# Optimization experiments

Measured on AMD Instinct MI355X. Metric: run time of the kernel, lower is better.

The kernel has to match this reference:

```python
import jax, jax.numpy as jnp
import numpy as np

N_HEADS = 8
N_POINTS = 4
LN_EPS = 1e-5


def _ln(x, g, b):
    m = jnp.mean(x, -1, keepdims=True)
    v = jnp.mean((x - m) ** 2, -1, keepdims=True)
    return (x - m) * jax.lax.rsqrt(v + LN_EPS) * g + b


def _mha(q, k, v, wq, bq, wk, bk, wv, bv, wo, bo):
    B, Lq, C = q.shape
    Dh = C // N_HEADS
    Q = (q @ wq.T + bq).reshape(B, Lq, N_HEADS, Dh)
    K = (k @ wk.T + bk).reshape(B, -1, N_HEADS, Dh)
    V = (v @ wv.T + bv).reshape(B, -1, N_HEADS, Dh)
    s = jnp.einsum('bqhd,bkhd->bhqk', Q, K) * (1.0 / float(np.sqrt(Dh)))
    a = jax.nn.softmax(s, -1)
    o = jnp.einsum('bhqk,bkhd->bqhd', a, V).reshape(B, Lq, C)
    return o @ wo.T + bo


def _ref_points(h, w, L):
    ry = jnp.linspace(0.5, h - 0.5, h) / h
    rx = jnp.linspace(0.5, w - 0.5, w) / w
    gy, gx = jnp.meshgrid(ry, rx, indexing='ij')
    ref = jnp.stack([gx.reshape(-1), gy.reshape(-1)], -1)[None]  # (1, h*w, 2)
    return jnp.broadcast_to(ref[:, :, None, :], (1, h * w, L, 2))


def _deform_core(value, shapes, starts, loc, aw):
    # value: (B, Len_in, H, Dh); loc: (B, Lq, H, L, P, 2); aw: (B, Lq, H, L, P)
    B, _, H, Dh = value.shape
    Lq, P = loc.shape[1], loc.shape[4]
    out = jnp.zeros((B, H, Lq, Dh), value.dtype)
    for l in range(shapes.shape[0]):
        Hl, Wl = int(shapes[l, 0]), int(shapes[l, 1])
        s = int(starts[l])
        v = value[:, s:s + Hl * Wl].transpose(0, 2, 1, 3)  # (B, H, Hl*Wl, Dh)
        # grid_sample(align_corners=False, padding_mode='zeros') pixel coords
        xl = loc[:, :, :, l, :, 0] * Wl - 0.5  # (B, Lq, H, P)
        yl = loc[:, :, :, l, :, 1] * Hl - 0.5
        x0 = jnp.floor(xl); y0 = jnp.floor(yl)
        fx = xl - x0; fy = yl - y0
        x0 = x0.astype(jnp.int32); y0 = y0.astype(jnp.int32)
        acc = jnp.zeros((B, H, Lq, P, Dh), value.dtype)
        for dy, dx in ((0, 0), (0, 1), (1, 0), (1, 1)):
            xi = x0 + dx; yi = y0 + dy
            wgt = (fx if dx else 1.0 - fx) * (fy if dy else 1.0 - fy)
            valid = ((xi >= 0) & (xi < Wl) & (yi >= 0) & (yi < Hl)).astype(value.dtype)
            idx = (jnp.clip(yi, 0, Hl - 1) * Wl + jnp.clip(xi, 0, Wl - 1))
            idx = idx.transpose(0, 2, 1, 3).reshape(B, H, Lq * P)
            g = jnp.take_along_axis(v, idx[..., None], axis=2).reshape(B, H, Lq, P, Dh)
            acc = acc + g * (wgt * valid).transpose(0, 2, 1, 3)[..., None]
        out = out + jnp.einsum('bhqpd,bqhp->bhqd', acc, aw[:, :, :, l])
    return out.transpose(0, 2, 1, 3).reshape(B, Lq, H * Dh)


def reference(tgt, query_pos, src, wq, bq, wk, bk, wv, bv, wo, bo, ln2_g, ln2_b,
              w_off, b_off, w_attn, b_attn, w_val, b_val, w_cout, b_cout,
              ln1_g, ln1_b, w1, b1, w2, b2, ln3_g, ln3_b,
              src_spatial_shapes, level_start_index, h, w):
    shapes = np.asarray(src_spatial_shapes)
    starts = np.asarray(level_start_index)
    h = int(h); w = int(w)
    L = shapes.shape[0]
    B, Lq, C = tgt.shape
    Dh = C // N_HEADS
    # --- self attention (post-LN residual) ---
    q = tgt + query_pos
    t2 = _mha(q, q, tgt, wq, bq, wk, bk, wv, bv, wo, bo)
    t = _ln(tgt + t2, ln2_g, ln2_b)
    # --- MSDeformAttn cross attention ---
    qc = t + query_pos
    value = (src @ w_val.T + b_val).reshape(B, -1, N_HEADS, Dh)
    off = (qc @ w_off.T + b_off).reshape(B, Lq, N_HEADS, L, N_POINTS, 2)
    aw = (qc @ w_attn.T + b_attn).reshape(B, Lq, N_HEADS, L * N_POINTS)
    aw = jax.nn.softmax(aw, -1).reshape(B, Lq, N_HEADS, L, N_POINTS)
    norm = jnp.stack([shapes[:, 1].astype(np.float32), shapes[:, 0].astype(np.float32)], -1)  # (L,2): (W,H)
    rp = _ref_points(h, w, L)  # (1, Lq, L, 2)
    loc = rp[:, :, None, :, None, :] + off / norm[None, None, None, :, None, :]
    samp = _deform_core(value, shapes, starts, loc, aw)
    t2 = samp @ w_cout.T + b_cout
    t = _ln(t + t2, ln1_g, ln1_b)
    # --- FFN ---
    t2 = jax.nn.relu(t @ w1.T + b1) @ w2.T + b2
    t = _ln(t + t2, ln3_g, ln3_b)
    return t


def setup_inputs() -> dict:
    key = jax.random.key(0)
    B, C, L, P, dff = 2, 256, 4, 4, 1024
    h = w = 48
    shapes = np.array([[48, 48], [24, 24], [12, 12], [6, 6]], np.int32)
    starts = np.array([0, 2304, 2880, 3024], np.int32)
    Len_in = 3060
    Lq = h * w
    ks = iter(jax.random.split(key, 40))
    def rn(shape, s=0.02):
        return jax.random.normal(next(ks), shape, jnp.float32) * s
    return dict(
        tgt=rn((B, Lq, C), 1.0), query_pos=rn((B, Lq, C), 1.0), src=rn((B, Len_in, C), 1.0),
        wq=rn((C, C)), bq=rn((C,)), wk=rn((C, C)), bk=rn((C,)), wv=rn((C, C)), bv=rn((C,)),
        wo=rn((C, C)), bo=rn((C,)),
        ln2_g=jnp.ones((C,)), ln2_b=jnp.zeros((C,)),
        w_off=rn((N_HEADS * L * P * 2, C)), b_off=rn((N_HEADS * L * P * 2,)),
        w_attn=rn((N_HEADS * L * P, C)), b_attn=rn((N_HEADS * L * P,)),
        w_val=rn((C, C)), b_val=rn((C,)), w_cout=rn((C, C)), b_cout=rn((C,)),
        ln1_g=jnp.ones((C,)), ln1_b=jnp.zeros((C,)),
        w1=rn((dff, C)), b1=rn((dff,)), w2=rn((C, dff)), b2=rn((C,)),
        ln3_g=jnp.ones((C,)), ln3_b=jnp.zeros((C,)),
        src_spatial_shapes=shapes, level_start_index=starts, h=h, w=w)
```

## Files before the change

kernel.cpp:

```cpp
#include <hip/hip_runtime.h>
#include <hip/hip_bf16.h>
#include <math.h>

typedef __hip_bfloat16 bf16;
typedef __attribute__((ext_vector_type(8))) short short8;
typedef __attribute__((ext_vector_type(4))) short short4v;
typedef __attribute__((ext_vector_type(4))) float f32x4;

static constexpr int B   = 2;
static constexpr int LQ  = 2304;
static constexpr int C   = 256;
static constexpr int NH  = 8;
static constexpr int DH  = 32;
static constexpr int NL  = 4;
static constexpr int NP  = 4;
static constexpr int LEN = 3060;
static constexpr int DFF = 1024;
static constexpr int MQ  = B * LQ;
static constexpr int MV  = B * LEN;
static constexpr int SZ1 = MQ * C;

#define MFMA16(a, b, c) __builtin_amdgcn_mfma_f32_16x16x32_bf16(a, b, c, 0, 0, 0)

__device__ __forceinline__ float ldf(const void* p, size_t i, int bf) {
  return bf ? __bfloat162float(((const bf16*)p)[i]) : ((const float*)p)[i];
}
__device__ __forceinline__ short fl2s(float v) {
  bf16 h = __float2bfloat16(v);
  return *(short*)&h;
}
__device__ __forceinline__ short fl2s_fast(float v) {
  union { float f; unsigned u; } x; x.f = v;
  return (short)((x.u + 0x8000u) >> 16);
}
__device__ __forceinline__ float s2fl(short s) {
  return __bfloat162float(*(bf16*)&s);
}
__device__ __forceinline__ int wire_is_bf16(const unsigned* gprobe) {
  return gprobe[0] == 0x3F803F80u;
}
__device__ __forceinline__ short8 add2bf(short8 a, short8 b) {
  short8 r;
#pragma unroll
  for (int j = 0; j < 8; ++j) r[j] = fl2s(s2fl(a[j]) + s2fl(b[j]));
  return r;
}

static constexpr int CVN = 20;
__device__ const int g_cvt_cnt[CVN] = {
  65536, 65536, 256, 256, 65536, 256, 65536, 256,
  65536, 32768, 256, 128, 65536, 256, 65536, 256,
  262144, 1024, 262144, 256};
__device__ const int g_cvt_off[CVN] = {
  0, 65536, 131072, 131328, 131584, 197120, 197376, 262912,
  263168, 328704, 361472, 361728, 361856, 427392, 427648, 493184,
  493440, 755584, 756608, 1018752};
static constexpr int CV_WQ = 0, CV_WK = 65536, CV_BQ = 131072, CV_BK = 131328;
static constexpr int CV_WV = 131584, CV_BV = 197120;
static constexpr int CV_WO = 197376, CV_BO = 262912;
static constexpr int CV_WOFF = 263168, CV_WATTN = 328704;
static constexpr int CV_BOFF = 361472, CV_BATTN = 361728;
static constexpr int CV_WVAL = 361856, CV_BVAL = 427392;
static constexpr int CV_WCOUT = 427648, CV_BCOUT = 493184;
static constexpr int CV_W1 = 493440, CV_B1 = 755584;
static constexpr int CV_W2 = 756608, CV_B2 = 1018752;
static constexpr int CV_TOTAL = 1019008;

struct CvtArgs { const void* p[22]; };

__global__ __launch_bounds__(256) void prep_all(CvtArgs a, const void* __restrict__ qpos,
                                                short* __restrict__ cvt,
                                                short* __restrict__ tgt16,
                                                short* __restrict__ q16,
                                                short* __restrict__ src16,
                                                const unsigned* __restrict__ gprobe) {
  if (wire_is_bf16(gprobe)) return;
  const int seg = blockIdx.y;
  const int cnt = (seg < 20) ? g_cvt_cnt[seg] : (seg == 20 ? SZ1 : MV * C);
  const int stride = gridDim.x * 256;
  for (int i = blockIdx.x * 256 + threadIdx.x; i < cnt; i += stride) {
    if (seg < 20) {
      cvt[g_cvt_off[seg] + i] = fl2s(((const float*)a.p[seg])[i]);
    } else if (seg == 20) {
      float t = ((const float*)a.p[20])[i];
      tgt16[i] = fl2s(t);
      q16[i] = fl2s(t + ((const float*)qpos)[i]);
    } else {
      src16[i] = fl2s(((const float*)a.p[21])[i]);
    }
  }
}

struct GemmJob {
  int Xmode;
  const short* Xbf; const void* Xwire; const void* Xwire2;
  const short* Wcvt; const short* bcvt;
  const void* Wwire; const void* bwire;
  void* Y;
  int M, N, K, ldY, col0, relu, out_mode, nblk_x;
  float qscale;
};
struct GemmBatch { GemmJob j[4]; int start[5]; int njobs; };

template <int MR>
__global__ __launch_bounds__(256) void gemm_mfma(GemmBatch nb,
                                                 const unsigned* __restrict__ gprobe) {
  constexpr int MT = MR / 64;
  const int fl = wire_is_bf16(gprobe);
  int id = blockIdx.x;
  int jj = 0;
  while (jj + 1 < nb.njobs && id >= nb.start[jj + 1]) ++jj;
  const GemmJob jb = nb.j[jj];
  const bool qcf = (jb.Xmode == 4) && fl;
  const short* Xsel = jb.Xbf;
  if ((jb.Xmode == 2 || jb.Xmode == 3) && fl) Xsel = (const short*)jb.Xwire;
  const short* Wsel = fl ? (const short*)jb.Wwire : jb.Wcvt;
  const short* bsel = fl ? (const short*)jb.bwire : jb.bcvt;
  const int local = id - nb.start[jj];
  const int bx = local % jb.nblk_x;
  const int by = local / jb.nblk_x;
  const int M = jb.M, N = jb.N, K = jb.K;

  __shared__ short Xs[MR][72];
  __shared__ short Ws[64][72];
  const int tid = threadIdx.x;
  const int wave = tid >> 6, lane = tid & 63;
  const int quad = lane >> 4, l16 = lane & 15;
  const int m0 = bx * MR, n0 = by * 64;
  f32x4 acc[MT][4];
#pragma unroll
  for (int mt = 0; mt < MT; ++mt)
#pragma unroll
    for (int nt = 0; nt < 4; ++nt) acc[mt][nt] = f32x4{0.f, 0.f, 0.f, 0.f};

  const int xrow = (MR == 128) ? (tid >> 1) : (tid >> 2);
  const int xcol = (MR == 128) ? ((tid & 1) * 32) : ((tid & 3) * 16);
  constexpr int XU = (MR == 128) ? 4 : 2;
  const int wrow = tid >> 2;
  const int wcol = (tid & 3) * 16;
  int xr = m0 + xrow; if (xr >= M) xr = M - 1;
  const short* xp = qcf ? nullptr : (Xsel + (size_t)xr * K);
  const short* tp = qcf ? ((const short*)jb.Xwire + (size_t)xr * K) : nullptr;
  const short* pp = qcf ? ((const short*)jb.Xwire2 + (size_t)xr * K) : nullptr;
  const short* wp = Wsel + (size_t)(n0 + wrow) * K;

  for (int k0 = 0; k0 < K; k0 += 64) {
    if (qcf) {
#pragma unroll
      for (int u = 0; u < XU; ++u) {
        short8 t8 = *(const short8*)(tp + k0 + xcol + u * 8);
        short8 p8 = *(const short8*)(pp + k0 + xcol + u * 8);
        *(short8*)&Xs[xrow][xcol + u * 8] = add2bf(t8, p8);
      }
    } else {
#pragma unroll
      for (int u = 0; u < XU; ++u)
        *(short8*)&Xs[xrow][xcol + u * 8] = *(const short8*)(xp + k0 + xcol + u * 8);
    }
    *(short8*)&Ws[wrow][wcol]     = *(const short8*)(wp + k0 + wcol);
    *(short8*)&Ws[wrow][wcol + 8] = *(const short8*)(wp + k0 + wcol + 8);
    __syncthreads();
#pragma unroll
    for (int kc = 0; kc < 2; ++kc) {
#pragma unroll
      for (int mt = 0; mt < MT; ++mt) {
        short8 a = *(const short8*)&Xs[wave * (16 * MT) + mt * 16 + l16][kc * 32 + quad * 8];
#pragma unroll
        for (int nt = 0; nt < 4; ++nt) {
          short8 b = *(const short8*)&Ws[nt * 16 + l16][kc * 32 + quad * 8];
          acc[mt][nt] = MFMA16(a, b, acc[mt][nt]);
        }
      }
    }
    __syncthreads();
  }

  if (jb.out_mode == 2) {
#pragma unroll
    for (int mt = 0; mt < MT; ++mt) {
      const int mbase = m0 + wave * (16 * MT) + mt * 16 + quad * 4;
      const int b = mbase / LQ;
      const int qb_ = mbase - b * LQ;
#pragma unroll
      for (int nt = 0; nt < 4; ++nt) {
        const int n = n0 + nt * 16 + l16;
        const float bv = s2fl(bsel[n]);
        short4v v4;
#pragma unroll
        for (int r = 0; r < 4; ++r) v4[r] = fl2s(acc[mt][nt][r] + bv);
        *(short4v*)((short*)jb.Y + (size_t)(b * 256 + n) * LQ + qb_) = v4;
      }
    }
    return;
  }
#pragma unroll
  for (int mt = 0; mt < MT; ++mt)
#pragma unroll
    for (int nt = 0; nt < 4; ++nt) {
      const int n = n0 + nt * 16 + l16;
      const float bv = s2fl(bsel[n]);
#pragma unroll
      for (int r = 0; r < 4; ++r) {
        const int m = m0 + wave * (16 * MT) + mt * 16 + quad * 4 + r;
        if (m < M) {
          float v = (acc[mt][nt][r] + bv) * jb.qscale;
          if (jb.relu) v = fmaxf(v, 0.f);
          if (jb.out_mode == 1)
            ((short*)jb.Y)[(size_t)m * jb.ldY + jb.col0 + n] = fl2s(v);
          else
            ((float*)jb.Y)[(size_t)m * jb.ldY + jb.col0 + n] = v;
        }
      }
    }
}

struct LnGemmArgs {
  const short* X;
  const short* Wcvt; const short* bcvt;
  const void* Wwire; const void* bwire;
  const void* R; int Rmode;
  const void* g; const void* be;
  float* Yf32; short* Y16; void* Yfinal;
  const void* pos; short* Yqc;
  int K;
};

__global__ __launch_bounds__(256) void gemm_ln(LnGemmArgs a,
                                               const unsigned* __restrict__ gprobe) {
  const int fl = wire_is_bf16(gprobe);
  const short* Wsel = fl ? (const short*)a.Wwire : a.Wcvt;
  const short* bsel = fl ? (const short*)a.bwire : a.bcvt;
  const int K = a.K;

  __shared__ short Xs[32][72];
  __shared__ short Ws[256][72];
  __shared__ float red[4][32][2];
  __shared__ float minv[32][2];

  const int tid = threadIdx.x;
  const int wave = tid >> 6, lane = tid & 63;
  const int quad = lane >> 4, l16 = lane & 15;
  const int m0 = blockIdx.x * 32;

  f32x4 acc[2][4];
#pragma unroll
  for (int mt = 0; mt < 2; ++mt)
#pragma unroll
    for (int nt = 0; nt < 4; ++nt) acc[mt][nt] = f32x4{0.f, 0.f, 0.f, 0.f};

  const int xrow = tid >> 3, xcol = (tid & 7) * 8;
  const int wrow = tid >> 2, wcol = (tid & 3) * 16;
  const short* xp = a.X + (size_t)(m0 + xrow) * K + xcol;

  for (int k0 = 0; k0 < K; k0 += 64) {
    *(short8*)&Xs[xrow][xcol] = *(const short8*)(xp + k0);
#pragma unroll
    for (int u = 0; u < 4; ++u) {
      const short* wp = Wsel + (size_t)(u * 64 + wrow) * K + k0 + wcol;
      *(short8*)&Ws[u * 64 + wrow][wcol]     = *(const short8*)(wp);
      *(short8*)&Ws[u * 64 + wrow][wcol + 8] = *(const short8*)(wp + 8);
    }
    __syncthreads();
#pragma unroll
    for (int kc = 0; kc < 2; ++kc)
#pragma unroll
      for (int mt = 0; mt < 2; ++mt) {
        short8 av = *(const short8*)&Xs[mt * 16 + l16][kc * 32 + quad * 8];
#pragma unroll
        for (int nt = 0; nt < 4; ++nt) {
          short8 bv = *(const short8*)&Ws[wave * 64 + nt * 16 + l16][kc * 32 + quad * 8];
          acc[mt][nt] = MFMA16(av, bv, acc[mt][nt]);
        }
      }
    __syncthreads();
  }

  float gc[4], bc[4], bb[4];
#pragma unroll
  for (int nt = 0; nt < 4; ++nt) {
    const int n = wave * 64 + nt * 16 + l16;
    gc[nt] = ldf(a.g, n, fl);
    bc[nt] = ldf(a.be, n, fl);
    bb[nt] = s2fl(bsel[n]);
  }
#pragma unroll
  for (int mt = 0; mt < 2; ++mt)
#pragma unroll
    for (int r = 0; r < 4; ++r) {
      const int rloc = mt * 16 + quad * 4 + r;
      const size_t row = (size_t)(m0 + rloc);
      float s = 0.f, s2 = 0.f;
#pragma unroll
      for (int nt = 0; nt < 4; ++nt) {
        const int n = wave * 64 + nt * 16 + l16;
        const size_t idx = row * C + n;
        const float rv = (a.Rmode == 1) ? ldf(a.R, idx, fl) : ((const float*)a.R)[idx];
        const float v = acc[mt][nt][r] + bb[nt] + rv;
        acc[mt][nt][r] = v;
        s += v;
        s2 += v * v;
      }
#pragma unroll
      for (int off = 8; off > 0; off >>= 1) {
        s  += __shfl_xor(s, off);
        s2 += __shfl_xor(s2, off);
      }
      if (l16 == 0) { red[wave][rloc][0] = s; red[wave][rloc][1] = s2; }
    }
  __syncthreads();
  if (tid < 32) {
    const float s  = red[0][tid][0] + red[1][tid][0] + red[2][tid][0] + red[3][tid][0];
    const float s2 = red[0][tid][1] + red[1][tid][1] + red[2][tid][1] + red[3][tid][1];
    const float mean = s * (1.f / C);
    const float var = fmaxf(s2 * (1.f / C) - mean * mean, 0.f);
    minv[tid][0] = mean;
    minv[tid][1] = rsqrtf(var + 1e-5f);
  }
  __syncthreads();
#pragma unroll
  for (int mt = 0; mt < 2; ++mt)
#pragma unroll
    for (int r = 0; r < 4; ++r) {
      const int rloc = mt * 16 + quad * 4 + r;
      const size_t row = (size_t)(m0 + rloc);
      const float mean = minv[rloc][0], inv = minv[rloc][1];
#pragma unroll
      for (int nt = 0; nt < 4; ++nt) {
        const int n = wave * 64 + nt * 16 + l16;
        const size_t idx = row * C + n;
        const float y = (acc[mt][nt][r] - mean) * inv * gc[nt] + bc[nt];
        if (a.Yfinal) {
          if (fl) ((short*)a.Yfinal)[idx] = fl2s(y);
          else    ((float*)a.Yfinal)[idx] = y;
        } else {
          if (a.Yf32) a.Yf32[idx] = y;
          if (a.Y16)  a.Y16[idx] = fl2s(y);
          if (a.Yqc)  a.Yqc[idx] = fl2s(y + ldf(a.pos, idx, fl));
        }
      }
    }
}

__global__ __launch_bounds__(256) void flash_attn(const short* __restrict__ QK,
                                                  const short* __restrict__ Vt,
                                                  short* __restrict__ Op) {
  constexpr int LDQK = 512;
  constexpr int NC = LQ / 64;
  constexpr int NQT = 3;
  const int qb = blockIdx.x;
  const int bh = blockIdx.y;
  const int b = bh >> 3, h = bh & 7;
  const int tid = threadIdx.x;
  const int wave = tid >> 6, lane = tid & 63;
  const int quad = lane >> 4, l16 = lane & 15;

  __shared__ short Ps[4][16][68];
  __shared__ float lsh[256];

  const int q0 = qb * 48;
  const size_t rowb = (size_t)(b * LQ);
  const short* kcol = QK + 256 + h * DH + quad * 8;
  const short* vt0 = Vt + (size_t)(b * 256 + h * 32 + l16) * LQ + quad * 8;
  const short* vt1 = Vt + (size_t)(b * 256 + h * 32 + 16 + l16) * LQ + quad * 8;

  short8 qfrag[NQT];
#pragma unroll
  for (int qt = 0; qt < NQT; ++qt)
    qfrag[qt] = *(const short8*)(QK + (rowb + q0 + qt * 16 + l16) * LDQK + h * DH + quad * 8);

  f32x4 o0[NQT], o1[NQT];
  float lrow[NQT];
#pragma unroll
  for (int qt = 0; qt < NQT; ++qt) {
    o0[qt] = f32x4{0.f, 0.f, 0.f, 0.f};
    o1[qt] = f32x4{0.f, 0.f, 0.f, 0.f};
    lrow[qt] = 0.f;
  }

  short8 kf[4], vf[4];
  {
    const int k0 = wave * 64;
#pragma unroll
    for (int kt = 0; kt < 4; ++kt)
      kf[kt] = *(const short8*)(kcol + (rowb + k0 + kt * 16 + l16) * LDQK);
    vf[0] = *(const short8*)(vt0 + k0);
    vf[1] = *(const short8*)(vt0 + k0 + 32);
    vf[2] = *(const short8*)(vt1 + k0);
    vf[3] = *(const short8*)(vt1 + k0 + 32);
  }

  for (int c = wave; c < NC; c += 4) {
    short8 kn[4], vn[4];
    if (c + 4 < NC) {
      const int k0n = (c + 4) * 64;
#pragma unroll
      for (int kt = 0; kt < 4; ++kt)
        kn[kt] = *(const short8*)(kcol + (rowb + k0n + kt * 16 + l16) * LDQK);
      vn[0] = *(const short8*)(vt0 + k0n);
      vn[1] = *(const short8*)(vt0 + k0n + 32);
      vn[2] = *(const short8*)(vt1 + k0n);
      vn[3] = *(const short8*)(vt1 + k0n + 32);
    }

#pragma unroll
    for (int qt = 0; qt < NQT; ++qt) {
      f32x4 s[4];
#pragma unroll
      for (int kt = 0; kt < 4; ++kt) {
        f32x4 z = {0.f, 0.f, 0.f, 0.f};
        s[kt] = MFMA16(kf[kt], qfrag[qt], z);
      }

      float ps = 0.f;
#pragma unroll
      for (int kt = 0; kt < 4; ++kt)
#pragma unroll
        for (int r = 0; r < 4; ++r) {
          float p = __expf(s[kt][r]);
          s[kt][r] = p;
          ps += p;
        }
      lrow[qt] += ps;

#pragma unroll
      for (int kt = 0; kt < 4; ++kt) {
        short4v pk;
#pragma unroll
        for (int r = 0; r < 4; ++r) pk[r] = fl2s_fast(s[kt][r]);
        *(short4v*)&Ps[wave][l16][kt * 16 + quad * 4] = pk;
      }

#pragma unroll
      for (int half = 0; half < 2; ++half) {
        short4v a0 = *(const short4v*)&Ps[wave][l16][half * 32 + quad * 8];
        short4v a1 = *(const short4v*)&Ps[wave][l16][half * 32 + quad * 8 + 4];
        short8 afrag;
#pragma unroll
        for (int j = 0; j < 4; ++j) { afrag[j] = a0[j]; afrag[4 + j] = a1[j]; }
        o0[qt] = MFMA16(afrag, vf[half], o0[qt]);
        o1[qt] = MFMA16(afrag, vf[2 + half], o1[qt]);
      }
    }

#pragma unroll
    for (int kt = 0; kt < 4; ++kt) { kf[kt] = kn[kt]; vf[kt] = vn[kt]; }
  }

  float* obuf = (float*)&Ps[0][0][0];
  for (int qt = 0; qt < NQT; ++qt) {
    __syncthreads();
    lsh[(wave * 4 + quad) * 16 + l16] = lrow[qt];
#pragma unroll
    for (int r = 0; r < 4; ++r) {
      const int q = quad * 4 + r;
      obuf[(wave * 16 + q) * 32 + l16] = o0[qt][r];
      obuf[(wave * 16 + q) * 32 + 16 + l16] = o1[qt][r];
    }
    __syncthreads();
#pragma unroll
    for (int e = tid; e < 512; e += 256) {
      const int q = e >> 5, d = e & 31;
      float lg = 0.f;
#pragma unroll
      for (int i = 0; i < 16; ++i) lg += lsh[i * 16 + q];
      float ov = 0.f;
#pragma unroll
      for (int w = 0; w < 4; ++w) ov += obuf[(w * 16 + q) * 32 + d];
      Op[(rowb + q0 + qt * 16 + q) * C + h * DH + d] = fl2s_fast(ov / lg);
    }
  }
}

__global__ __launch_bounds__(256) void deform_kern(const short* __restrict__ value,
                                                   const float* __restrict__ oa,
                                                   const int* __restrict__ shapes,
                                                   const int* __restrict__ starts,
                                                   const int* __restrict__ hp,
                                                   const int* __restrict__ wp,
                                                   short* __restrict__ samp) {
  const int bq = blockIdx.x * 4 + (threadIdx.x >> 6);
  const int b = bq / LQ, q = bq % LQ;
  const int lane = threadIdx.x & 63;
  const int h_ = lane >> 3;
  const int d0 = (lane & 7) * 4;

  const int w0 = *wp, h0 = *hp;
  const int qx = q % w0, qy = q / w0;
  const float refx = (qx + 0.5f) / (float)w0;
  const float refy = (qy + 0.5f) / (float)h0;

  const float* offp = oa + (size_t)bq * 384 + h_ * 32;
  const float* awraw = oa + (size_t)bq * 384 + 256 + h_ * 16;

  float e[16];
  float mm = -1e30f;
#pragma unroll
  for (int j = 0; j < 16; ++j) mm = fmaxf(mm, awraw[j]);
  float ssum = 0.f;
#pragma unroll
  for (int j = 0; j < 16; ++j) {
    e[j] = __expf(awraw[j] - mm);
    ssum += e[j];
  }
  const float sinv = 1.f / ssum;

  float acc0 = 0.f, acc1 = 0.f, acc2 = 0.f, acc3 = 0.f;
  for (int l = 0; l < NL; ++l) {
    const int Hl = shapes[l * 2 + 0];
    const int Wl = shapes[l * 2 + 1];
    const int st = starts[l];
    const short* vbase = value + ((size_t)(b * LEN + st)) * C + h_ * DH + d0;
#pragma unroll
    for (int p = 0; p < NP; ++p) {
      const float ox = offp[l * 8 + p * 2 + 0];
      const float oy = offp[l * 8 + p * 2 + 1];
      const float a = e[l * 4 + p] * sinv;
      const float xl = refx * Wl + ox - 0.5f;
      const float yl = refy * Hl + oy - 0.5f;
      const float x0f = floorf(xl), y0f = floorf(yl);
      const float fx = xl - x0f, fy = yl - y0f;
      const int x0 = (int)x0f, y0 = (int)y0f;
#pragma unroll
      for (int corner = 0; corner < 4; ++corner) {
        const int dx = corner & 1, dy = corner >> 1;
        const int xi = x0 + dx, yi = y0 + dy;
        const float wx = dx ? fx : 1.f - fx;
        const float wy = dy ? fy : 1.f - fy;
        const bool valid = (xi >= 0) & (xi < Wl) & (yi >= 0) & (yi < Hl);
        if (valid) {
          const float w = a * wx * wy;
          short4v v4 = *(const short4v*)(vbase + (size_t)(yi * Wl + xi) * C);
          acc0 += w * s2fl(v4[0]);
          acc1 += w * s2fl(v4[1]);
          acc2 += w * s2fl(v4[2]);
          acc3 += w * s2fl(v4[3]);
        }
      }
    }
  }
  short4v out;
  out[0] = fl2s(acc0); out[1] = fl2s(acc1); out[2] = fl2s(acc2); out[3] = fl2s(acc3);
  *(short4v*)(samp + (size_t)bq * C + h_ * DH + d0) = out;
}

extern "C" void kernel_launch(void* const* d_in, const int* in_sizes, int n_in,
                              void* d_out, int out_size, void* d_ws, size_t ws_size,
                              hipStream_t stream) {
  const void* tgt       = d_in[0];
  const void* query_pos = d_in[1];
  const void* src       = d_in[2];
  const void* wq = d_in[3];  const void* bq = d_in[4];
  const void* wk = d_in[5];  const void* bk = d_in[6];
  const void* wv = d_in[7];  const void* bv = d_in[8];
  const void* wo = d_in[9];  const void* bo = d_in[10];
  const void* ln2_g = d_in[11]; const void* ln2_b = d_in[12];
  const void* w_off = d_in[13]; const void* b_off = d_in[14];
  const void* w_attn = d_in[15]; const void* b_attn = d_in[16];
  const void* w_val = d_in[17]; const void* b_val = d_in[18];
  const void* w_cout = d_in[19]; const void* b_cout = d_in[20];
  const void* ln1_g = d_in[21]; const void* ln1_b = d_in[22];
  const void* w1 = d_in[23]; const void* b1 = d_in[24];
  const void* w2 = d_in[25]; const void* b2 = d_in[26];
  const void* ln3_g = d_in[27]; const void* ln3_b = d_in[28];
  const int* shapes = (const int*)d_in[29];
  const int* starts = (const int*)d_in[30];
  const int* hp = (const int*)d_in[31];
  const int* wp = (const int*)d_in[32];
  const unsigned* gprobe = (const unsigned*)ln2_g;

  short* cvt    = (short*)((char*)d_ws + 256);
  short* tgt16  = cvt + CV_TOTAL;
  short* q16    = tgt16 + SZ1;
  short* src16  = q16 + SZ1;
  short* qk_out = src16 + (size_t)MV * C;
  short* vt16   = qk_out + (size_t)MQ * 512;
  short* ao16   = vt16 + SZ1;
  short* valb   = ao16 + SZ1;
  short* ffn1   = valb + (size_t)MV * C;
  short* t1_16  = ffn1 + (size_t)MQ * DFF;
  float* t_32   = (float*)(t1_16 + SZ1);
  float* t1_32  = t_32 + SZ1;
  float* oa     = t1_32 + SZ1;

  const float scale = 1.f / sqrtf((float)DH);
  const dim3 blk(256);
  const int NX128 = MQ / 128;
  const int NX64  = MQ / 64;
  const int NX32  = MQ / 32;
  const int NXV   = (MV + 127) / 128;

  CvtArgs ca;
  ca.p[0] = wq;  ca.p[1] = wk;  ca.p[2] = bq;  ca.p[3] = bk;
  ca.p[4] = wv;  ca.p[5] = bv;  ca.p[6] = wo;  ca.p[7] = bo;
  ca.p[8] = w_off; ca.p[9] = w_attn; ca.p[10] = b_off; ca.p[11] = b_attn;
  ca.p[12] = w_val; ca.p[13] = b_val; ca.p[14] = w_cout; ca.p[15] = b_cout;
  ca.p[16] = w1; ca.p[17] = b1; ca.p[18] = w2; ca.p[19] = b2;
  ca.p[20] = tgt; ca.p[21] = src;
  prep_all<<<dim3(96, 22), blk, 0, stream>>>(ca, query_pos, cvt, tgt16, q16, src16, gprobe);

  {
    GemmBatch nb;
    nb.njobs = 4;
    nb.j[0] = {4, q16, tgt, query_pos, cvt + CV_WQ, cvt + CV_BQ, wq, bq, qk_out,
               MQ, 256, 256, 512, 0, 0, 1, NX128, scale};
    nb.j[1] = {4, q16, tgt, query_pos, cvt + CV_WK, cvt + CV_BK, wk, bk, qk_out,
               MQ, 256, 256, 512, 256, 0, 1, NX128, 1.f};
    nb.j[2] = {2, tgt16, tgt, nullptr, cvt + CV_WV, cvt + CV_BV, wv, bv, vt16,
               MQ, 256, 256, 0, 0, 0, 2, NX128, 1.f};
    nb.j[3] = {3, src16, src, nullptr, cvt + CV_WVAL, cvt + CV_BVAL, w_val, b_val, valb,
               MV, 256, 256, 256, 0, 0, 1, NXV, 1.f};
    nb.start[0] = 0;
    nb.start[1] = NX128 * 4;
    nb.start[2] = nb.start[1] + NX128 * 4;
    nb.start[3] = nb.start[2] + NX128 * 4;
    nb.start[4] = nb.start[3] + NXV * 4;
    gemm_mfma<128><<<nb.start[4], blk, 0, stream>>>(nb, gprobe);
  }
  flash_attn<<<dim3(LQ / 48, B * NH), blk, 0, stream>>>(qk_out, vt16, ao16);

  {
    LnGemmArgs a;
    a.X = ao16; a.Wcvt = cvt + CV_WO; a.bcvt = cvt + CV_BO; a.Wwire = wo; a.bwire = bo;
    a.R = tgt; a.Rmode = 1; a.g = ln2_g; a.be = ln2_b;
    a.Yf32 = t_32; a.Y16 = nullptr; a.Yfinal = nullptr;
    a.pos = query_pos; a.Yqc = q16;
    a.K = 256;
    gemm_ln<<<NX32, blk, 0, stream>>>(a, gprobe);
  }

  {
    GemmBatch nb;
    nb.njobs = 2;
    nb.j[0] = {0, q16, nullptr, nullptr, cvt + CV_WOFF, cvt + CV_BOFF, w_off, b_off, oa,
               MQ, 256, 256, 384, 0, 0, 0, NX64, 1.f};
    nb.j[1] = {0, q16, nullptr, nullptr, cvt + CV_WATTN, cvt + CV_BATTN, w_attn, b_attn, oa,
               MQ, 128, 256, 384, 256, 0, 0, NX64, 1.f};
    nb.start[0] = 0;
    nb.start[1] = NX64 * 4;
    nb.start[2] = nb.start[1] + NX64 * 2;
    gemm_mfma<64><<<nb.start[2], blk, 0, stream>>>(nb, gprobe);
  }
  deform_kern<<<MQ / 4, blk, 0, stream>>>(valb, oa, shapes, starts, hp, wp, ao16);

  {
    LnGemmArgs a;
    a.X = ao16; a.Wcvt = cvt + CV_WCOUT; a.bcvt = cvt + CV_BCOUT; a.Wwire = w_cout; a.bwire = b_cout;
    a.R = t_32; a.Rmode = 2; a.g = ln1_g; a.be = ln1_b;
    a.Yf32 = t1_32; a.Y16 = t1_16; a.Yfinal = nullptr;
    a.pos = nullptr; a.Yqc = nullptr;
    a.K = 256;
    gemm_ln<<<NX32, blk, 0, stream>>>(a, gprobe);
  }

  {
    GemmBatch nb;
    nb.njobs = 1;
    nb.j[0] = {0, t1_16, nullptr, nullptr, cvt + CV_W1, cvt + CV_B1, w1, b1, ffn1,
               MQ, 1024, 256, 1024, 0, 1, 1, NX128, 1.f};
    nb.start[0] = 0; nb.start[1] = NX128 * 16;
    gemm_mfma<128><<<nb.start[1], blk, 0, stream>>>(nb, gprobe);
  }
  {
    LnGemmArgs a;
    a.X = ffn1; a.Wcvt = cvt + CV_W2; a.bcvt = cvt + CV_B2; a.Wwire = w2; a.bwire = b2;
    a.R = t1_32; a.Rmode = 2; a.g = ln3_g; a.be = ln3_b;
    a.Yf32 = nullptr; a.Y16 = nullptr; a.Yfinal = d_out;
    a.pos = nullptr; a.Yqc = nullptr;
    a.K = 1024;
    gemm_ln<<<NX32, blk, 0, stream>>>(a, gprobe);
  }
}
```

Before: 290.5 us.

## Fold fp32-to-bf16 conversion into GEMM loads and double-buffer LN GEMM

Removes the separate prep kernel that converted weights, biases and activations to bf16. The GEMM and GEMM+LayerNorm kernels now read fp32 inputs directly and convert while staging into shared memory. This saves a launch and a full write and re-read of the converted buffers, but every weight tile is converted again in each block. The LN GEMM also moves to 16-row tiles with K=32 double-buffered shared-memory stages, which doubles its grid and overlaps the next load with the current MFMA work.

```diff
diff --git a/kernel.cpp b/kernel.cpp
--- a/kernel.cpp
+++ b/kernel.cpp
@@ -39,62 +39,19 @@
 __device__ __forceinline__ int wire_is_bf16(const unsigned* gprobe) {
   return gprobe[0] == 0x3F803F80u;
 }
+__device__ __forceinline__ float ldbias(const void* b, int n, int fl) {
+  return fl ? s2fl(((const short*)b)[n]) : s2fl(fl2s(((const float*)b)[n]));
+}
 __device__ __forceinline__ short8 add2bf(short8 a, short8 b) {
   short8 r;
 #pragma unroll
   for (int j = 0; j < 8; ++j) r[j] = fl2s(s2fl(a[j]) + s2fl(b[j]));
   return r;
-}
-
-static constexpr int CVN = 20;
-__device__ const int g_cvt_cnt[CVN] = {
-  65536, 65536, 256, 256, 65536, 256, 65536, 256,
-  65536, 32768, 256, 128, 65536, 256, 65536, 256,
-  262144, 1024, 262144, 256};
-__device__ const int g_cvt_off[CVN] = {
-  0, 65536, 131072, 131328, 131584, 197120, 197376, 262912,
-  263168, 328704, 361472, 361728, 361856, 427392, 427648, 493184,
-  493440, 755584, 756608, 1018752};
-static constexpr int CV_WQ = 0, CV_WK = 65536, CV_BQ = 131072, CV_BK = 131328;
-static constexpr int CV_WV = 131584, CV_BV = 197120;
-static constexpr int CV_WO = 197376, CV_BO = 262912;
-static constexpr int CV_WOFF = 263168, CV_WATTN = 328704;
-static constexpr int CV_BOFF = 361472, CV_BATTN = 361728;
-static constexpr int CV_WVAL = 361856, CV_BVAL = 427392;
-static constexpr int CV_WCOUT = 427648, CV_BCOUT = 493184;
-static constexpr int CV_W1 = 493440, CV_B1 = 755584;
-static constexpr int CV_W2 = 756608, CV_B2 = 1018752;
-static constexpr int CV_TOTAL = 1019008;
-
-struct CvtArgs { const void* p[22]; };
-
-__global__ __launch_bounds__(256) void prep_all(CvtArgs a, const void* __restrict__ qpos,
-                                                short* __restrict__ cvt,
-                                                short* __restrict__ tgt16,
-                                                short* __restrict__ q16,
-                                                short* __restrict__ src16,
-                                                const unsigned* __restrict__ gprobe) {
-  if (wire_is_bf16(gprobe)) return;
-  const int seg = blockIdx.y;
-  const int cnt = (seg < 20) ? g_cvt_cnt[seg] : (seg == 20 ? SZ1 : MV * C);
-  const int stride = gridDim.x * 256;
-  for (int i = blockIdx.x * 256 + threadIdx.x; i < cnt; i += stride) {
-    if (seg < 20) {
-      cvt[g_cvt_off[seg] + i] = fl2s(((const float*)a.p[seg])[i]);
-    } else if (seg == 20) {
-      float t = ((const float*)a.p[20])[i];
-      tgt16[i] = fl2s(t);
-      q16[i] = fl2s(t + ((const float*)qpos)[i]);
-    } else {
-      src16[i] = fl2s(((const float*)a.p[21])[i]);
-    }
-  }
 }
 
 struct GemmJob {
   int Xmode;
   const short* Xbf; const void* Xwire; const void* Xwire2;
-  const short* Wcvt; const short* bcvt;
   const void* Wwire; const void* bwire;
   void* Y;
   int M, N, K, ldY, col0, relu, out_mode, nblk_x;
@@ -111,11 +68,6 @@
   int jj = 0;
   while (jj + 1 < nb.njobs && id >= nb.start[jj + 1]) ++jj;
   const GemmJob jb = nb.j[jj];
-  const bool qcf = (jb.Xmode == 4) && fl;
-  const short* Xsel = jb.Xbf;
-  if ((jb.Xmode == 2 || jb.Xmode == 3) && fl) Xsel = (const short*)jb.Xwire;
-  const short* Wsel = fl ? (const short*)jb.Wwire : jb.Wcvt;
-  const short* bsel = fl ? (const short*)jb.bwire : jb.bcvt;
   const int local = id - nb.start[jj];
   const int bx = local % jb.nblk_x;
   const int by = local / jb.nblk_x;
@@ -139,26 +91,69 @@
   const int wrow = tid >> 2;
   const int wcol = (tid & 3) * 16;
   int xr = m0 + xrow; if (xr >= M) xr = M - 1;
-  const short* xp = qcf ? nullptr : (Xsel + (size_t)xr * K);
-  const short* tp = qcf ? ((const short*)jb.Xwire + (size_t)xr * K) : nullptr;
-  const short* pp = qcf ? ((const short*)jb.Xwire2 + (size_t)xr * K) : nullptr;
-  const short* wp = Wsel + (size_t)(n0 + wrow) * K;
+
+  const short* xp16 = nullptr; const float* xpf = nullptr;
+  const short* tp16 = nullptr; const short* pp16 = nullptr;
+  const float* tpf  = nullptr; const float* ppf  = nullptr;
+  if (jb.Xmode == 0) {
+    xp16 = jb.Xbf + (size_t)xr * K;
+  } else if (jb.Xmode == 2) {
+    if (fl) xp16 = (const short*)jb.Xwire + (size_t)xr * K;
+    else    xpf  = (const float*)jb.Xwire + (size_t)xr * K;
+  } else {
+    if (fl) { tp16 = (const short*)jb.Xwire + (size_t)xr * K;
+              pp16 = (const short*)jb.Xwire2 + (size_t)xr * K; }
+    else    { tpf  = (const float*)jb.Xwire + (size_t)xr * K;
+              ppf  = (const float*)jb.Xwire2 + (size_t)xr * K; }
+  }
+  const short* wp16 = (const short*)jb.Wwire;
+  const float* wpf  = (const float*)jb.Wwire;
+  const size_t wro = (size_t)(n0 + wrow) * K;
 
   for (int k0 = 0; k0 < K; k0 += 64) {
-    if (qcf) {
+    if (xp16) {
+#pragma unroll
+      for (int u = 0; u < XU; ++u)
+        *(short8*)&Xs[xrow][xcol + u * 8] = *(const short8*)(xp16 + k0 + xcol + u * 8);
+    } else if (xpf) {
 #pragma unroll
       for (int u = 0; u < XU; ++u) {
-        short8 t8 = *(const short8*)(tp + k0 + xcol + u * 8);
-        short8 p8 = *(const short8*)(pp + k0 + xcol + u * 8);
+        const float* s = xpf + k0 + xcol + u * 8;
+        short8 r;
+#pragma unroll
+        for (int j = 0; j < 8; ++j) r[j] = fl2s(s[j]);
+        *(short8*)&Xs[xrow][xcol + u * 8] = r;
+      }
+    } else if (tp16) {
+#pragma unroll
+      for (int u = 0; u < XU; ++u) {
+        short8 t8 = *(const short8*)(tp16 + k0 + xcol + u * 8);
+        short8 p8 = *(const short8*)(pp16 + k0 + xcol + u * 8);
         *(short8*)&Xs[xrow][xcol + u * 8] = add2bf(t8, p8);
       }
     } else {
 #pragma unroll
-      for (int u = 0; u < XU; ++u)
-        *(short8*)&Xs[xrow][xcol + u * 8] = *(const short8*)(xp + k0 + xcol + u * 8);
-    }
-    *(short8*)&Ws[wrow][wcol]     = *(const short8*)(wp + k0 + wcol);
-    *(short8*)&Ws[wrow][wcol + 8] = *(const short8*)(wp + k0 + wcol + 8);
+      for (int u = 0; u < XU; ++u) {
+        const float* t = tpf + k0 + xcol + u * 8;
+        const float* p = ppf + k0 + xcol + u * 8;
+        short8 r;
+#pragma unroll
+        for (int j = 0; j < 8; ++j) r[j] = fl2s(t[j] + p[j]);
+        *(short8*)&Xs[xrow][xcol + u * 8] = r;
+      }
+    }
+    if (fl) {
+      const short* wp = wp16 + wro + k0 + wcol;
+      *(short8*)&Ws[wrow][wcol]     = *(const short8*)(wp);
+      *(short8*)&Ws[wrow][wcol + 8] = *(const short8*)(wp + 8);
+    } else {
+      const float* wp = wpf + wro + k0 + wcol;
+      short8 w0, w1;
+#pragma unroll
+      for (int j = 0; j < 8; ++j) { w0[j] = fl2s(wp[j]); w1[j] = fl2s(wp[8 + j]); }
+      *(short8*)&Ws[wrow][wcol]     = w0;
+      *(short8*)&Ws[wrow][wcol + 8] = w1;
+    }
     __syncthreads();
 #pragma unroll
     for (int kc = 0; kc < 2; ++kc) {
@@ -184,7 +179,7 @@
 #pragma unroll
       for (int nt = 0; nt < 4; ++nt) {
         const int n = n0 + nt * 16 + l16;
-        const float bv = s2fl(bsel[n]);
+        const float bv = ldbias(jb.bwire, n, fl);
         short4v v4;
 #pragma unroll
         for (int r = 0; r < 4; ++r) v4[r] = fl2s(acc[mt][nt][r] + bv);
@@ -198,7 +193,7 @@
 #pragma unroll
     for (int nt = 0; nt < 4; ++nt) {
       const int n = n0 + nt * 16 + l16;
-      const float bv = s2fl(bsel[n]);
+      const float bv = ldbias(jb.bwire, n, fl);
 #pragma unroll
       for (int r = 0; r < 4; ++r) {
         const int m = m0 + wave * (16 * MT) + mt * 16 + quad * 4 + r;
@@ -216,7 +211,6 @@
 
 struct LnGemmArgs {
   const short* X;
-  const short* Wcvt; const short* bcvt;
   const void* Wwire; const void* bwire;
   const void* R; int Rmode;
   const void* g; const void* be;
@@ -228,51 +222,60 @@
 __global__ __launch_bounds__(256) void gemm_ln(LnGemmArgs a,
                                                const unsigned* __restrict__ gprobe) {
   const int fl = wire_is_bf16(gprobe);
-  const short* Wsel = fl ? (const short*)a.Wwire : a.Wcvt;
-  const short* bsel = fl ? (const short*)a.bwire : a.bcvt;
   const int K = a.K;
-
-  __shared__ short Xs[32][72];
-  __shared__ short Ws[256][72];
-  __shared__ float red[4][32][2];
-  __shared__ float minv[32][2];
+  const int NT = K >> 5;
+
+  __shared__ short Xs[2][16][40];
+  __shared__ short Ws[2][256][40];
+  __shared__ float red[4][16][2];
+  __shared__ float minv[16][2];
 
   const int tid = threadIdx.x;
   const int wave = tid >> 6, lane = tid & 63;
   const int quad = lane >> 4, l16 = lane & 15;
-  const int m0 = blockIdx.x * 32;
-
-  f32x4 acc[2][4];
-#pragma unroll
-  for (int mt = 0; mt < 2; ++mt)
-#pragma unroll
-    for (int nt = 0; nt < 4; ++nt) acc[mt][nt] = f32x4{0.f, 0.f, 0.f, 0.f};
-
-  const int xrow = tid >> 3, xcol = (tid & 7) * 8;
-  const int wrow = tid >> 2, wcol = (tid & 3) * 16;
-  const short* xp = a.X + (size_t)(m0 + xrow) * K + xcol;
-
-  for (int k0 = 0; k0 < K; k0 += 64) {
-    *(short8*)&Xs[xrow][xcol] = *(const short8*)(xp + k0);
+  const int m0 = blockIdx.x * 16;
+
+  f32x4 acc[4];
+#pragma unroll
+  for (int nt = 0; nt < 4; ++nt) acc[nt] = f32x4{0.f, 0.f, 0.f, 0.f};
+
+  const int xrow = (tid & 63) >> 2, xcol = (tid & 3) * 8;
+  const int wr0 = tid >> 2, wc0 = (tid & 3) * 8;
+  const short* xpr = a.X + (size_t)(m0 + xrow) * K + xcol;
+  const short* wp16 = (const short*)a.Wwire;
+  const float* wpf  = (const float*)a.Wwire;
+
+  auto STAGE = [&](int buf, int k0) {
+    if (tid < 64)
+      *(short8*)&Xs[buf][xrow][xcol] = *(const short8*)(xpr + k0);
 #pragma unroll
     for (int u = 0; u < 4; ++u) {
-      const short* wp = Wsel + (size_t)(u * 64 + wrow) * K + k0 + wcol;
-      *(short8*)&Ws[u * 64 + wrow][wcol]     = *(const short8*)(wp);
-      *(short8*)&Ws[u * 64 + wrow][wcol + 8] = *(const short8*)(wp + 8);
+      const int rr = u * 64 + wr0;
+      if (fl) {
+        *(short8*)&Ws[buf][rr][wc0] = *(const short8*)(wp16 + (size_t)rr * K + k0 + wc0);
+      } else {
+        const float* wp = wpf + (size_t)rr * K + k0 + wc0;
+        short8 w;
+#pragma unroll
+        for (int j = 0; j < 8; ++j) w[j] = fl2s(wp[j]);
+        *(short8*)&Ws[buf][rr][wc0] = w;
+      }
+    }
+  };
+
+  STAGE(0, 0);
+  __syncthreads();
+  int cur = 0;
+  for (int t = 0; t < NT; ++t) {
+    if (t + 1 < NT) STAGE(cur ^ 1, (t + 1) << 5);
+    short8 av = *(const short8*)&Xs[cur][l16][quad * 8];
+#pragma unroll
+    for (int nt = 0; nt < 4; ++nt) {
+      short8 bv = *(const short8*)&Ws[cur][wave * 64 + nt * 16 + l16][quad * 8];
+      acc[nt] = MFMA16(av, bv, acc[nt]);
     }
     __syncthreads();
-#pragma unroll
-    for (int kc = 0; kc < 2; ++kc)
-#pragma unroll
-      for (int mt = 0; mt < 2; ++mt) {
-        short8 av = *(const short8*)&Xs[mt * 16 + l16][kc * 32 + quad * 8];
-#pragma unroll
-        for (int nt = 0; nt < 4; ++nt) {
-          short8 bv = *(const short8*)&Ws[wave * 64 + nt * 16 + l16][kc * 32 + quad * 8];
-          acc[mt][nt] = MFMA16(av, bv, acc[mt][nt]);
-        }
-      }
-    __syncthreads();
+    cur ^= 1;
   }
 
   float gc[4], bc[4], bb[4];
@@ -281,34 +284,32 @@
     const int n = wave * 64 + nt * 16 + l16;
     gc[nt] = ldf(a.g, n, fl);
     bc[nt] = ldf(a.be, n, fl);
-    bb[nt] = s2fl(bsel[n]);
-  }
-#pragma unroll
-  for (int mt = 0; mt < 2; ++mt)
-#pragma unroll
-    for (int r = 0; r < 4; ++r) {
-      const int rloc = mt * 16 + quad * 4 + r;
-      const size_t row = (size_t)(m0 + rloc);
-      float s = 0.f, s2 = 0.f;
-#pragma unroll
-      for (int nt = 0; nt < 4; ++nt) {
-        const int n = wave * 64 + nt * 16 + l16;
-        const size_t idx = row * C + n;
-        const float rv = (a.Rmode == 1) ? ldf(a.R, idx, fl) : ((const float*)a.R)[idx];
-        const float v = acc[mt][nt][r] + bb[nt] + rv;
-        acc[mt][nt][r] = v;
-        s += v;
-        s2 += v * v;
-      }
-#pragma unroll
-      for (int off = 8; off > 0; off >>= 1) {
-        s  += __shfl_xor(s, off);
-        s2 += __shfl_xor(s2, off);
-      }
-      if (l16 == 0) { red[wave][rloc][0] = s; red[wave][rloc][1] = s2; }
-    }
+    bb[nt] = ldbias(a.bwire, n, fl);
+  }
+#pragma unroll
+  for (int r = 0; r < 4; ++r) {
+    const int rloc = quad * 4 + r;
+    const size_t row = (size_t)(m0 + rloc);
+    float s = 0.f, s2 = 0.f;
+#pragma unroll
+    for (int nt = 0; nt < 4; ++nt) {
+      const int n = wave * 64 + nt * 16 + l16;
+      const size_t idx = row * C + n;
+      const float rv = (a.Rmode == 1) ? ldf(a.R, idx, fl) : ((const float*)a.R)[idx];
+      const float v = acc[nt][r] + bb[nt] + rv;
+      acc[nt][r] = v;
+      s += v;
+      s2 += v * v;
+    }
+#pragma unroll
+    for (int off = 8; off > 0; off >>= 1) {
+      s  += __shfl_xor(s, off);
+      s2 += __shfl_xor(s2, off);
+    }
+    if (l16 == 0) { red[wave][rloc][0] = s; red[wave][rloc][1] = s2; }
+  }
   __syncthreads();
-  if (tid < 32) {
+  if (tid < 16) {
     const float s  = red[0][tid][0] + red[1][tid][0] + red[2][tid][0] + red[3][tid][0];
     const float s2 = red[0][tid][1] + red[1][tid][1] + red[2][tid][1] + red[3][tid][1];
     const float mean = s * (1.f / C);
@@ -318,27 +319,25 @@
   }
   __syncthreads();
 #pragma unroll
-  for (int mt = 0; mt < 2; ++mt)
-#pragma unroll
-    for (int r = 0; r < 4; ++r) {
-      const int rloc = mt * 16 + quad * 4 + r;
-      const size_t row = (size_t)(m0 + rloc);
-      const float mean = minv[rloc][0], inv = minv[rloc][1];
-#pragma unroll
-      for (int nt = 0; nt < 4; ++nt) {
-        const int n = wave * 64 + nt * 16 + l16;
-        const size_t idx = row * C + n;
-        const float y = (acc[mt][nt][r] - mean) * inv * gc[nt] + bc[nt];
-        if (a.Yfinal) {
-          if (fl) ((short*)a.Yfinal)[idx] = fl2s(y);
-          else    ((float*)a.Yfinal)[idx] = y;
-        } else {
-          if (a.Yf32) a.Yf32[idx] = y;
-          if (a.Y16)  a.Y16[idx] = fl2s(y);
-          if (a.Yqc)  a.Yqc[idx] = fl2s(y + ldf(a.pos, idx, fl));
-        }
-      }
-    }
+  for (int r = 0; r < 4; ++r) {
+    const int rloc = quad * 4 + r;
+    const size_t row = (size_t)(m0 + rloc);
+    const float mean = minv[rloc][0], inv = minv[rloc][1];
+#pragma unroll
+    for (int nt = 0; nt < 4; ++nt) {
+      const int n = wave * 64 + nt * 16 + l16;
+      const size_t idx = row * C + n;
+      const float y = (acc[nt][r] - mean) * inv * gc[nt] + bc[nt];
+      if (a.Yfinal) {
+        if (fl) ((short*)a.Yfinal)[idx] = fl2s(y);
+        else    ((float*)a.Yfinal)[idx] = y;
+      } else {
+        if (a.Yf32) a.Yf32[idx] = y;
+        if (a.Y16)  a.Y16[idx] = fl2s(y);
+        if (a.Yqc)  a.Yqc[idx] = fl2s(y + ldf(a.pos, idx, fl));
+      }
+    }
+  }
 }
 
 __global__ __launch_bounds__(256) void flash_attn(const short* __restrict__ QK,
@@ -568,11 +567,8 @@
   const int* wp = (const int*)d_in[32];
   const unsigned* gprobe = (const unsigned*)ln2_g;
 
-  short* cvt    = (short*)((char*)d_ws + 256);
-  short* tgt16  = cvt + CV_TOTAL;
-  short* q16    = tgt16 + SZ1;
-  short* src16  = q16 + SZ1;
-  short* qk_out = src16 + (size_t)MV * C;
+  short* q16    = (short*)((char*)d_ws + 256);
+  short* qk_out = q16 + SZ1;
   short* vt16   = qk_out + (size_t)MQ * 512;
   short* ao16   = vt16 + SZ1;
   short* valb   = ao16 + SZ1;
@@ -586,28 +582,19 @@
   const dim3 blk(256);
   const int NX128 = MQ / 128;
   const int NX64  = MQ / 64;
-  const int NX32  = MQ / 32;
+  const int NX16  = MQ / 16;
   const int NXV   = (MV + 127) / 128;
-
-  CvtArgs ca;
-  ca.p[0] = wq;  ca.p[1] = wk;  ca.p[2] = bq;  ca.p[3] = bk;
-  ca.p[4] = wv;  ca.p[5] = bv;  ca.p[6] = wo;  ca.p[7] = bo;
-  ca.p[8] = w_off; ca.p[9] = w_attn; ca.p[10] = b_off; ca.p[11] = b_attn;
-  ca.p[12] = w_val; ca.p[13] = b_val; ca.p[14] = w_cout; ca.p[15] = b_cout;
-  ca.p[16] = w1; ca.p[17] = b1; ca.p[18] = w2; ca.p[19] = b2;
-  ca.p[20] = tgt; ca.p[21] = src;
-  prep_all<<<dim3(96, 22), blk, 0, stream>>>(ca, query_pos, cvt, tgt16, q16, src16, gprobe);
 
   {
     GemmBatch nb;
     nb.njobs = 4;
-    nb.j[0] = {4, q16, tgt, query_pos, cvt + CV_WQ, cvt + CV_BQ, wq, bq, qk_out,
+    nb.j[0] = {4, nullptr, tgt, query_pos, wq, bq, qk_out,
                MQ, 256, 256, 512, 0, 0, 1, NX128, scale};
-    nb.j[1] = {4, q16, tgt, query_pos, cvt + CV_WK, cvt + CV_BK, wk, bk, qk_out,
+    nb.j[1] = {4, nullptr, tgt, query_pos, wk, bk, qk_out,
                MQ, 256, 256, 512, 256, 0, 1, NX128, 1.f};
-    nb.j[2] = {2, tgt16, tgt, nullptr, cvt + CV_WV, cvt + CV_BV, wv, bv, vt16,
+    nb.j[2] = {2, nullptr, tgt, nullptr, wv, bv, vt16,
                MQ, 256, 256, 0, 0, 0, 2, NX128, 1.f};
-    nb.j[3] = {3, src16, src, nullptr, cvt + CV_WVAL, cvt + CV_BVAL, w_val, b_val, valb,
+    nb.j[3] = {2, nullptr, src, nullptr, w_val, b_val, valb,
                MV, 256, 256, 256, 0, 0, 1, NXV, 1.f};
     nb.start[0] = 0;
     nb.start[1] = NX128 * 4;
@@ -620,20 +607,20 @@
 
   {
     LnGemmArgs a;
-    a.X = ao16; a.Wcvt = cvt + CV_WO; a.bcvt = cvt + CV_BO; a.Wwire = wo; a.bwire = bo;
+    a.X = ao16; a.Wwire = wo; a.bwire = bo;
     a.R = tgt; a.Rmode = 1; a.g = ln2_g; a.be = ln2_b;
     a.Yf32 = t_32; a.Y16 = nullptr; a.Yfinal = nullptr;
     a.pos = query_pos; a.Yqc = q16;
     a.K = 256;
-    gemm_ln<<<NX32, blk, 0, stream>>>(a, gprobe);
+    gemm_ln<<<NX16, blk, 0, stream>>>(a, gprobe);
   }
 
   {
     GemmBatch nb;
     nb.njobs = 2;
-    nb.j[0] = {0, q16, nullptr, nullptr, cvt + CV_WOFF, cvt + CV_BOFF, w_off, b_off, oa,
+    nb.j[0] = {0, q16, nullptr, nullptr, w_off, b_off, oa,
                MQ, 256, 256, 384, 0, 0, 0, NX64, 1.f};
-    nb.j[1] = {0, q16, nullptr, nullptr, cvt + CV_WATTN, cvt + CV_BATTN, w_attn, b_attn, oa,
+    nb.j[1] = {0, q16, nullptr, nullptr, w_attn, b_attn, oa,
                MQ, 128, 256, 384, 256, 0, 0, NX64, 1.f};
     nb.start[0] = 0;
     nb.start[1] = NX64 * 4;
@@ -644,29 +631,29 @@
 
   {
     LnGemmArgs a;
-    a.X = ao16; a.Wcvt = cvt + CV_WCOUT; a.bcvt = cvt + CV_BCOUT; a.Wwire = w_cout; a.bwire = b_cout;
+    a.X = ao16; a.Wwire = w_cout; a.bwire = b_cout;
     a.R = t_32; a.Rmode = 2; a.g = ln1_g; a.be = ln1_b;
     a.Yf32 = t1_32; a.Y16 = t1_16; a.Yfinal = nullptr;
     a.pos = nullptr; a.Yqc = nullptr;
     a.K = 256;
-    gemm_ln<<<NX32, blk, 0, stream>>>(a, gprobe);
+    gemm_ln<<<NX16, blk, 0, stream>>>(a, gprobe);
   }
 
   {
     GemmBatch nb;
     nb.njobs = 1;
-    nb.j[0] = {0, t1_16, nullptr, nullptr, cvt + CV_W1, cvt + CV_B1, w1, b1, ffn1,
+    nb.j[0] = {0, t1_16, nullptr, nullptr, w1, b1, ffn1,
                MQ, 1024, 256, 1024, 0, 1, 1, NX128, 1.f};
     nb.start[0] = 0; nb.start[1] = NX128 * 16;
     gemm_mfma<128><<<nb.start[1], blk, 0, stream>>>(nb, gprobe);
   }
   {
     LnGemmArgs a;
-    a.X = ffn1; a.Wcvt = cvt + CV_W2; a.bcvt = cvt + CV_B2; a.Wwire = w2; a.bwire = b2;
+    a.X = ffn1; a.Wwire = w2; a.bwire = b2;
     a.R = t1_32; a.Rmode = 2; a.g = ln3_g; a.be = ln3_b;
     a.Yf32 = nullptr; a.Y16 = nullptr; a.Yfinal = d_out;
     a.pos = nullptr; a.Yqc = nullptr;
     a.K = 1024;
-    gemm_ln<<<NX32, blk, 0, stream>>>(a, gprobe);
-  }
-}
+    gemm_ln<<<NX16, blk, 0, stream>>>(a, gprobe);
+  }
+}
```

New measurement: 336.0 us. +15.7%, slower.
